# Performance work log

Hardware: AMD Instinct MI355X
Metric: run time of the kernel (lower is better)

## Reference

```python
import jax, jax.numpy as jnp
import numpy as np

B, T, D, K = 32, 1024, 256, 1024


def setup_inputs() -> dict:
    key = jax.random.key(0)
    k1, k2 = jax.random.split(key)
    x = jax.random.normal(k1, (B, T, D), dtype=jnp.float32)
    # nn.Embedding init: uniform(-1/emb_size, 1/emb_size)
    embedding = jax.random.uniform(k2, (K, D), dtype=jnp.float32,
                                   minval=-1.0 / K, maxval=1.0 / K)
    return {"x": x, "embedding": embedding}


def reference(x, embedding):
    # x: [B, T, D], embedding: [K, D]
    Bx, Tx, Dx = x.shape
    flat = x.reshape(-1, Dx)  # [N, D]
    dist = (jnp.sum(embedding * embedding, axis=1)
            - 2.0 * flat @ embedding.T
            + jnp.sum(flat * flat, axis=1, keepdims=True))
    quantized_idx = jnp.argmin(dist, axis=1).reshape(Bx, Tx)  # [B, T] int
    # onehot @ W  ==  gather rows of W
    embed_idx = embedding[quantized_idx]  # [B, T, D]
    # straight-through estimator
    embed_idx_qx = x + jax.lax.stop_gradient(embed_idx - x)
    return embed_idx, embed_idx_qx, quantized_idx
```

## Files before the change

kernel.cpp:

```cpp
#include <hip/hip_runtime.h>
#include <math.h>

#define N_ROWS 32768
#define DIM    256
#define KCODES 1024
#define DELTA  5.0e-4f
#define CSPLIT 4
#define TILES  (KCODES / 16 / CSPLIT)

typedef float f32x4 __attribute__((ext_vector_type(4)));
typedef short s16x8 __attribute__((ext_vector_type(8)));

__device__ inline unsigned short bf_rne(float f) {
    unsigned u = __float_as_uint(f);
    return (unsigned short)((u + 0x7FFFu + ((u >> 16) & 1u)) >> 16);
}

__device__ inline void ins4(float v, int ix, float (&tv)[4], int (&ti)[4]) {
#pragma unroll
    for (int s = 0; s < 4; ++s) {
        bool better = (v < tv[s]) || (v == tv[s] && ix < ti[s]);
        float dv = better ? tv[s] : v;
        int   di = better ? ti[s] : ix;
        tv[s] = better ? v : tv[s];
        ti[s] = better ? ix : ti[s];
        v = dv; ix = di;
    }
}

__device__ __forceinline__ void gl_lds16(const void* gp, void* lp) {
    __builtin_amdgcn_global_load_lds(
        (__attribute__((address_space(1))) void*)(void*)gp,
        (__attribute__((address_space(3))) void*)lp, 16, 0, 0);
}

__global__ __launch_bounds__(256) void prep_kernel(const float* __restrict__ E,
                                                   float* __restrict__ e2,
                                                   unsigned short* __restrict__ Eh) {
    __shared__ float sq[4][260];
    const int wave = threadIdx.x >> 6;
    const int lane = threadIdx.x & 63;
    const int row = blockIdx.x * 4 + wave;
    const float4* rp = (const float4*)(E + (size_t)row * DIM);
    float4 v = rp[lane];
    sq[wave][lane * 4 + 0] = v.x * v.x;
    sq[wave][lane * 4 + 1] = v.y * v.y;
    sq[wave][lane * 4 + 2] = v.z * v.z;
    sq[wave][lane * 4 + 3] = v.w * v.w;
    float fs[4] = {v.x, v.y, v.z, v.w};
    ushort4 hv;
    unsigned short* hp = (unsigned short*)&hv;
#pragma unroll
    for (int j = 0; j < 4; ++j) hp[j] = bf_rne(fs[j]);
    *(ushort4*)(Eh + (size_t)row * DIM + lane * 4) = hv;
    if (lane < 8) {
#pragma clang fp contract(off)
        const int j = lane;
        float rA = sq[wave][j];
#pragma unroll
        for (int m = 1; m < 16; ++m) rA += sq[wave][8 * m + j];
        float rB = sq[wave][128 + j];
#pragma unroll
        for (int m = 1; m < 16; ++m) rB += sq[wave][128 + 8 * m + j];
        rA = rA + __shfl_xor(rA, 1, 64); rA = rA + __shfl_xor(rA, 2, 64);
        rA = rA + __shfl_xor(rA, 4, 64);
        rB = rB + __shfl_xor(rB, 1, 64); rB = rB + __shfl_xor(rB, 2, 64);
        rB = rB + __shfl_xor(rB, 4, 64);
        if (j == 0) e2[row] = rA + rB;
    }
}

__device__ float x2_exact(const float* __restrict__ xr) {
#pragma clang fp contract(off)
    float rr[16];
#pragma unroll
    for (int j = 0; j < 8; ++j) {
        float a = xr[j] * xr[j];
#pragma unroll
        for (int m = 1; m < 16; ++m) { float t = xr[8 * m + j]; float s = t * t; a += s; }
        rr[j] = a;
        float b = xr[128 + j] * xr[128 + j];
#pragma unroll
        for (int m = 1; m < 16; ++m) { float t = xr[128 + 8 * m + j]; float s = t * t; b += s; }
        rr[8 + j] = b;
    }
    float a01 = rr[0] + rr[1], a23 = rr[2] + rr[3];
    float a45 = rr[4] + rr[5], a67 = rr[6] + rr[7];
    float A = (a01 + a23) + (a45 + a67);
    float b01 = rr[8] + rr[9], b23 = rr[10] + rr[11];
    float b45 = rr[12] + rr[13], b67 = rr[14] + rr[15];
    float Bt = (b01 + b23) + (b45 + b67);
    return A + Bt;
}

__global__ __launch_bounds__(256) void vq_screen_kernel(const float* __restrict__ X,
                                                        const unsigned short* __restrict__ Eh,
                                                        const float* __restrict__ e2g,
                                                        float* __restrict__ topv,
                                                        unsigned short* __restrict__ topi) {
    __shared__ __align__(16) short buf[3][4096];
    __shared__ __align__(16) float e2_lds[256];

    const int tid  = threadIdx.x;
    const int w    = tid >> 6;
    const int l    = tid & 63;
    const int c16  = l & 15;
    const int quad = l >> 4;
    const int bx   = blockIdx.x;
    const int h    = bx & (CSPLIT - 1);
    const int rb   = bx >> 2;
    const int row0 = rb * 64;
    const int cbase = h * (KCODES / CSPLIT);

    if (w == 0) gl_lds16(e2g + cbase + l * 4, &e2_lds[0]);

    s16x8 xh[8];
    {
        const float* xrow = X + (size_t)(row0 + w * 16 + c16) * DIM + quad * 8;
#pragma unroll
        for (int ks = 0; ks < 8; ++ks) {
            float4 f0 = *(const float4*)(xrow + ks * 32);
            float4 f1 = *(const float4*)(xrow + ks * 32 + 4);
            float fs[8] = {f0.x, f0.y, f0.z, f0.w, f1.x, f1.y, f1.z, f1.w};
#pragma unroll
            for (int j = 0; j < 8; ++j) xh[ks][j] = (short)bf_rne(fs[j]);
        }
    }

    const int rot = rb & (TILES - 1);
    auto stage = [&](int t) {
        const int ct = (t + rot) & (TILES - 1);
        const unsigned short* Ehc =
            Eh + (size_t)(cbase + ct * 16 + c16) * DIM + quad * 8;
        short* bp = &buf[t % 3][0];
#pragma unroll
        for (int gg = 0; gg < 2; ++gg) {
            const int ks = w + gg * 4;
            gl_lds16(Ehc + ks * 32, bp + ks * 512);
        }
    };

    stage(0);
    stage(1);

    float tva[4];
    int   tia[4];
#pragma unroll
    for (int s = 0; s < 4; ++s) { tva[s] = INFINITY; tia[s] = 0x7fffffff; }

    for (int t = 0; t < TILES; ++t) {
        asm volatile("s_waitcnt vmcnt(2)" ::: "memory");
        __builtin_amdgcn_s_barrier();
        __builtin_amdgcn_sched_barrier(0);
        if (t < TILES - 2) stage(t + 2);

        const int ct = (t + rot) & (TILES - 1);
        const short* bp = &buf[t % 3][0];
        s16x8 ch[8];
#pragma unroll
        for (int ks = 0; ks < 8; ++ks)
            ch[ks] = *(const s16x8*)(bp + ks * 512 + l * 8);

        f32x4 ce = {0.f, 0.f, 0.f, 0.f};
        f32x4 co = {0.f, 0.f, 0.f, 0.f};
#pragma unroll
        for (int ks = 0; ks < 8; ks += 2) {
            ce = __builtin_amdgcn_mfma_f32_16x16x32_bf16(ch[ks],     xh[ks],     ce, 0, 0, 0);
            co = __builtin_amdgcn_mfma_f32_16x16x32_bf16(ch[ks + 1], xh[ks + 1], co, 0, 0, 0);
        }
        f32x4 e2v = *(const f32x4*)&e2_lds[ct * 16 + quad * 4];
#pragma unroll
        for (int r = 0; r < 4; ++r) {
            const int code = cbase + ct * 16 + quad * 4 + r;
            ins4(fmaf(-2.0f, ce[r] + co[r], e2v[r]), code, tva, tia);
        }
    }

#pragma unroll
    for (int st = 16; st <= 32; st <<= 1) {
        float ov[4]; int oi[4];
#pragma unroll
        for (int s = 0; s < 4; ++s) {
            ov[s] = __shfl_xor(tva[s], st, 64);
            oi[s] = __shfl_xor(tia[s], st, 64);
        }
#pragma unroll
        for (int s = 0; s < 4; ++s) ins4(ov[s], oi[s], tva, tia);
    }

    if (quad == 0) {
        const int r = row0 + w * 16 + c16;
        const size_t o = ((size_t)h * N_ROWS + r) * 4;
#pragma unroll
        for (int s = 0; s < 4; ++s) {
            topv[o + s] = tva[s];
            topi[o + s] = (unsigned short)tia[s];
        }
    }
}

__global__ __launch_bounds__(256) void decide_gather_kernel(const float* __restrict__ X,
                                                            const float* __restrict__ E,
                                                            const float* __restrict__ e2g,
                                                            const float* __restrict__ topv,
                                                            const unsigned short* __restrict__ topi,
                                                            float* __restrict__ out0,
                                                            float* __restrict__ out1,
                                                            float* __restrict__ out2) {
    __shared__ int sidx[64];
    const int tid  = threadIdx.x;
    const int row0 = blockIdx.x * 64;
    if (tid < 64) {
        const int r = row0 + tid;
        float tv[4]; int ti[4];
#pragma unroll
        for (int s = 0; s < 4; ++s) { tv[s] = INFINITY; ti[s] = 0x7fffffff; }
#pragma unroll
        for (int hh = 0; hh < CSPLIT; ++hh) {
            const size_t o = ((size_t)hh * N_ROWS + r) * 4;
#pragma unroll
            for (int s = 0; s < 4; ++s) ins4(topv[o + s], (int)topi[o + s], tv, ti);
        }

        int best = ti[0];
        if (!(tv[1] > tv[0] + DELTA)) {
            const float* xr = X + (size_t)r * DIM;
            const float x2v = x2_exact(xr);
            float bq = INFINITY; int bi = 0x7fffffff;
            for (int cnd = 0; cnd < 4; ++cnd) {
                if (tv[cnd] <= tv[0] + DELTA) {
                    const int k = ti[cnd];
                    const float* er = E + (size_t)k * DIM;
                    float dot = 0.f;
                    for (int d = 0; d < DIM; d += 4) {
                        float4 xv = *(const float4*)(xr + d);
                        float4 ev = *(const float4*)(er + d);
                        dot = fmaf(xv.x, ev.x, dot);
                        dot = fmaf(xv.y, ev.y, dot);
                        dot = fmaf(xv.z, ev.z, dot);
                        dot = fmaf(xv.w, ev.w, dot);
                    }
                    float t1 = e2g[k] - 2.0f * dot;
                    float q  = t1 + x2v;
                    if (q < bq || (q == bq && k < bi)) { bq = q; bi = k; }
                }
            }
            best = bi;
        }
        sidx[tid] = best;
        out2[r] = (float)best;
    }
    __syncthreads();
#pragma unroll
    for (int it = 0; it < 16; ++it) {
        int f = tid + it * 256;
        int rr = f >> 6;
        int pp = f & 63;
        int ix = sidx[rr];
        float4 v = *(const float4*)(E + (size_t)ix * DIM + pp * 4);
        size_t o = (size_t)(row0 + rr) * DIM + (size_t)pp * 4;
        *(float4*)(out0 + o) = v;
        *(float4*)(out1 + o) = v;
    }
}

extern "C" void kernel_launch(void* const* d_in, const int* in_sizes, int n_in,
                              void* d_out, int out_size, void* d_ws, size_t ws_size,
                              hipStream_t stream) {
    const float* X = (const float*)d_in[0];
    const float* E = (const float*)d_in[1];

    float* e2 = (float*)d_ws;
    unsigned short* Eh = (unsigned short*)(e2 + KCODES);
    float* topv = (float*)(Eh + KCODES * DIM);
    unsigned short* topi =
        (unsigned short*)(topv + (size_t)CSPLIT * N_ROWS * 4);

    float* out0 = (float*)d_out;
    float* out1 = out0 + (size_t)N_ROWS * DIM;
    float* out2 = out1 + (size_t)N_ROWS * DIM;

    prep_kernel<<<dim3(KCODES / 4), dim3(256), 0, stream>>>(E, e2, Eh);
    vq_screen_kernel<<<dim3((N_ROWS / 64) * CSPLIT), dim3(256), 0, stream>>>(X, Eh, e2,
                                                                             topv, topi);
    decide_gather_kernel<<<dim3(N_ROWS / 64), dim3(256), 0, stream>>>(X, E, e2,
                                                                      topv, topi,
                                                                      out0, out1, out2);
}
```

Before: 193.1 us.

## Precompute bf16 X in prep kernel and double code split to eight

```diff
diff --git a/kernel.cpp b/kernel.cpp
--- a/kernel.cpp
+++ b/kernel.cpp
@@ -5,7 +5,7 @@
 #define DIM    256
 #define KCODES 1024
 #define DELTA  5.0e-4f
-#define CSPLIT 4
+#define CSPLIT 8
 #define TILES  (KCODES / 16 / CSPLIT)
 
 typedef float f32x4 __attribute__((ext_vector_type(4)));
@@ -35,38 +35,52 @@
 }
 
 __global__ __launch_bounds__(256) void prep_kernel(const float* __restrict__ E,
+                                                   const float* __restrict__ X,
                                                    float* __restrict__ e2,
-                                                   unsigned short* __restrict__ Eh) {
+                                                   unsigned short* __restrict__ Eh,
+                                                   unsigned short* __restrict__ Xh) {
     __shared__ float sq[4][260];
     const int wave = threadIdx.x >> 6;
     const int lane = threadIdx.x & 63;
-    const int row = blockIdx.x * 4 + wave;
-    const float4* rp = (const float4*)(E + (size_t)row * DIM);
-    float4 v = rp[lane];
-    sq[wave][lane * 4 + 0] = v.x * v.x;
-    sq[wave][lane * 4 + 1] = v.y * v.y;
-    sq[wave][lane * 4 + 2] = v.z * v.z;
-    sq[wave][lane * 4 + 3] = v.w * v.w;
-    float fs[4] = {v.x, v.y, v.z, v.w};
-    ushort4 hv;
-    unsigned short* hp = (unsigned short*)&hv;
-#pragma unroll
-    for (int j = 0; j < 4; ++j) hp[j] = bf_rne(fs[j]);
-    *(ushort4*)(Eh + (size_t)row * DIM + lane * 4) = hv;
-    if (lane < 8) {
+    if (blockIdx.x < KCODES / 4) {
+        const int row = blockIdx.x * 4 + wave;
+        const float4* rp = (const float4*)(E + (size_t)row * DIM);
+        float4 v = rp[lane];
+        sq[wave][lane * 4 + 0] = v.x * v.x;
+        sq[wave][lane * 4 + 1] = v.y * v.y;
+        sq[wave][lane * 4 + 2] = v.z * v.z;
+        sq[wave][lane * 4 + 3] = v.w * v.w;
+        float fs[4] = {v.x, v.y, v.z, v.w};
+        ushort4 hv;
+        unsigned short* hp = (unsigned short*)&hv;
+#pragma unroll
+        for (int j = 0; j < 4; ++j) hp[j] = bf_rne(fs[j]);
+        *(ushort4*)(Eh + (size_t)row * DIM + lane * 4) = hv;
+        if (lane < 8) {
 #pragma clang fp contract(off)
-        const int j = lane;
-        float rA = sq[wave][j];
-#pragma unroll
-        for (int m = 1; m < 16; ++m) rA += sq[wave][8 * m + j];
-        float rB = sq[wave][128 + j];
-#pragma unroll
-        for (int m = 1; m < 16; ++m) rB += sq[wave][128 + 8 * m + j];
-        rA = rA + __shfl_xor(rA, 1, 64); rA = rA + __shfl_xor(rA, 2, 64);
-        rA = rA + __shfl_xor(rA, 4, 64);
-        rB = rB + __shfl_xor(rB, 1, 64); rB = rB + __shfl_xor(rB, 2, 64);
-        rB = rB + __shfl_xor(rB, 4, 64);
-        if (j == 0) e2[row] = rA + rB;
+            const int j = lane;
+            float rA = sq[wave][j];
+#pragma unroll
+            for (int m = 1; m < 16; ++m) rA += sq[wave][8 * m + j];
+            float rB = sq[wave][128 + j];
+#pragma unroll
+            for (int m = 1; m < 16; ++m) rB += sq[wave][128 + 8 * m + j];
+            rA = rA + __shfl_xor(rA, 1, 64); rA = rA + __shfl_xor(rA, 2, 64);
+            rA = rA + __shfl_xor(rA, 4, 64);
+            rB = rB + __shfl_xor(rB, 1, 64); rB = rB + __shfl_xor(rB, 2, 64);
+            rB = rB + __shfl_xor(rB, 4, 64);
+            if (j == 0) e2[row] = rA + rB;
+        }
+    } else {
+        const int row = (blockIdx.x - KCODES / 4) * 4 + wave;
+        const float4* rp = (const float4*)(X + (size_t)row * DIM);
+        float4 v = rp[lane];
+        float fs[4] = {v.x, v.y, v.z, v.w};
+        ushort4 hv;
+        unsigned short* hp = (unsigned short*)&hv;
+#pragma unroll
+        for (int j = 0; j < 4; ++j) hp[j] = bf_rne(fs[j]);
+        *(ushort4*)(Xh + (size_t)row * DIM + lane * 4) = hv;
     }
 }
 
@@ -93,13 +107,13 @@
     return A + Bt;
 }
 
-__global__ __launch_bounds__(256) void vq_screen_kernel(const float* __restrict__ X,
+__global__ __launch_bounds__(256) void vq_screen_kernel(const unsigned short* __restrict__ Xh,
                                                         const unsigned short* __restrict__ Eh,
                                                         const float* __restrict__ e2g,
                                                         float* __restrict__ topv,
                                                         unsigned short* __restrict__ topi) {
     __shared__ __align__(16) short buf[3][4096];
-    __shared__ __align__(16) float e2_lds[256];
+    __shared__ __align__(16) float e2_lds[KCODES / CSPLIT];
 
     const int tid  = threadIdx.x;
     const int w    = tid >> 6;
@@ -108,24 +122,9 @@
     const int quad = l >> 4;
     const int bx   = blockIdx.x;
     const int h    = bx & (CSPLIT - 1);
-    const int rb   = bx >> 2;
+    const int rb   = bx >> 3;
     const int row0 = rb * 64;
     const int cbase = h * (KCODES / CSPLIT);
-
-    if (w == 0) gl_lds16(e2g + cbase + l * 4, &e2_lds[0]);
-
-    s16x8 xh[8];
-    {
-        const float* xrow = X + (size_t)(row0 + w * 16 + c16) * DIM + quad * 8;
-#pragma unroll
-        for (int ks = 0; ks < 8; ++ks) {
-            float4 f0 = *(const float4*)(xrow + ks * 32);
-            float4 f1 = *(const float4*)(xrow + ks * 32 + 4);
-            float fs[8] = {f0.x, f0.y, f0.z, f0.w, f1.x, f1.y, f1.z, f1.w};
-#pragma unroll
-            for (int j = 0; j < 8; ++j) xh[ks][j] = (short)bf_rne(fs[j]);
-        }
-    }
 
     const int rot = rb & (TILES - 1);
     auto stage = [&](int t) {
@@ -142,6 +141,17 @@
 
     stage(0);
     stage(1);
+
+    s16x8 xh[8];
+    {
+        const unsigned short* xrow =
+            Xh + (size_t)(row0 + w * 16 + c16) * DIM + quad * 8;
+#pragma unroll
+        for (int ks = 0; ks < 8; ++ks) xh[ks] = *(const s16x8*)(xrow + ks * 32);
+    }
+    if (tid < KCODES / CSPLIT) e2_lds[tid] = e2g[cbase + tid];
+
+    __syncthreads();
 
     float tva[4];
     int   tia[4];
@@ -272,7 +282,8 @@
 
     float* e2 = (float*)d_ws;
     unsigned short* Eh = (unsigned short*)(e2 + KCODES);
-    float* topv = (float*)(Eh + KCODES * DIM);
+    unsigned short* Xh = Eh + (size_t)KCODES * DIM;
+    float* topv = (float*)(Xh + (size_t)N_ROWS * DIM);
     unsigned short* topi =
         (unsigned short*)(topv + (size_t)CSPLIT * N_ROWS * 4);
 
@@ -280,8 +291,9 @@
     float* out1 = out0 + (size_t)N_ROWS * DIM;
     float* out2 = out1 + (size_t)N_ROWS * DIM;
 
-    prep_kernel<<<dim3(KCODES / 4), dim3(256), 0, stream>>>(E, e2, Eh);
-    vq_screen_kernel<<<dim3((N_ROWS / 64) * CSPLIT), dim3(256), 0, stream>>>(X, Eh, e2,
+    prep_kernel<<<dim3(KCODES / 4 + N_ROWS / 4), dim3(256), 0, stream>>>(E, X, e2,
+                                                                         Eh, Xh);
+    vq_screen_kernel<<<dim3((N_ROWS / 64) * CSPLIT), dim3(256), 0, stream>>>(Xh, Eh, e2,
                                                                              topv, topi);
     decide_gather_kernel<<<dim3(N_ROWS / 64), dim3(256), 0, stream>>>(X, E, e2,
                                                                       topv, topi,
```

Result: slower. 201.7 us (+4.4%).
